# Performance work log

Measured on AMD Instinct MI355X. Metric: run time of the kernel, lower is better.

## Reference

```python
import jax, jax.numpy as jnp
import numpy as np

B, N, F_IN, F_OUT = 8, 2048, 64, 64
NEG = -9.0e15  # matches torch's -9000000000000000.0 mask value


def setup_inputs() -> dict:
    key = jax.random.key(0)
    ks = jax.random.split(key, 12)
    stdv1 = 1.0 / np.sqrt(F_IN)
    stdv2 = 1.0 / np.sqrt(2 * F_OUT)
    x = jax.random.normal(ks[0], (B, N, F_IN), dtype=jnp.float32)
    adj = jax.random.randint(ks[1], (B, N, N), 0, 2).astype(jnp.int32)
    identity = jnp.broadcast_to(jnp.eye(N, dtype=jnp.int32), (B, N, N))
    def unif(k, shape, s):
        return jax.random.uniform(k, shape, jnp.float32, -s, s)
    return {
        "x": x, "adj": adj, "identity": identity,
        "W1": unif(ks[2], (F_OUT, F_IN), stdv1), "b1": unif(ks[3], (F_OUT,), stdv1),
        "a1": unif(ks[4], (1, 2 * F_OUT), stdv2), "ab1": unif(ks[5], (1,), stdv2),
        "W2": unif(ks[6], (F_OUT, F_IN), stdv1), "b2": unif(ks[7], (F_OUT,), stdv1),
        "a2": unif(ks[8], (1, 2 * F_OUT), stdv2), "ab2": unif(ks[9], (1,), stdv2),
    }


def _gat_layer(x, mask, W, b, a, ab):
    # linear1
    h = jnp.einsum('bnf,of->bno', x, W) + b                     # [B,N,Fo]
    Fo = h.shape[-1]
    # linear2 on concat(h_i, h_j) decomposes: e_ij = relu(h_i.a1 + h_j.a2 + ab)
    s1 = h @ a[0, :Fo]                                          # [B,N]
    s2 = h @ a[0, Fo:]                                          # [B,N]
    e = jax.nn.relu(s1[:, :, None] + s2[:, None, :] + ab[0])    # [B,N,N]
    e = jnp.where(mask > 0, e, NEG)
    att = jax.nn.softmax(e, axis=2)                             # [B,N,N]
    return jnp.einsum('bnm,bmf->bnf', att, h)                   # dropout p=0 / eval


def reference(x, adj, identity, W1, b1, a1, ab1, W2, b2, a2, ab2):
    out1 = _gat_layer(x, adj, W1, b1, a1, ab1)
    out2 = _gat_layer(x, identity, W2, b2, a2, ab2)
    return out1 + out2
```

## Files before the change

kernel.cpp:

```cpp
#include <hip/hip_runtime.h>


#define DEVI __device__ __forceinline__

typedef __attribute__((ext_vector_type(8))) short short8;
typedef __attribute__((ext_vector_type(4))) float floatx4;

DEVI unsigned short f2bf(float x) {
    unsigned u = __builtin_bit_cast(unsigned, x);
    unsigned r = u + 0x7FFFu + ((u >> 16) & 1u);
    return (unsigned short)(r >> 16);
}

DEVI short8 pack8(const float* v) {
    short8 r;
#pragma unroll
    for (int i = 0; i < 8; ++i) r[i] = (short)f2bf(v[i]);
    return r;
}

DEVI unsigned cvt_pk_bf16(float lo, float hi) {
    unsigned r;
    asm("v_cvt_pk_bf16_f32 %0, %1, %2" : "=v"(r) : "v"(lo), "v"(hi));
    return r;
}

__global__ __launch_bounds__(256) void k_prep(
    const float* __restrict__ x, const float* __restrict__ W1,
    const float* __restrict__ b1, const float* __restrict__ a1,
    const float* __restrict__ ab1,
    unsigned short* __restrict__ hT1,
    float* __restrict__ t1,
    float* __restrict__ s2a)
{
    __shared__ __align__(16) unsigned short hstage[64][72];
    const int tid = threadIdx.x;
    const int w = tid >> 6, lane = tid & 63;
    const int g = lane >> 4, r15 = lane & 15;
    const int blockRow = blockIdx.x * 64;
    const int rowbase = blockRow + w * 16;

    float xa[8], xb[8];
    const float* xrow = x + (long)(rowbase + r15) * 64;
#pragma unroll
    for (int e = 0; e < 8; ++e) { xa[e] = xrow[g * 8 + e]; xb[e] = xrow[32 + g * 8 + e]; }
    short8 A0 = pack8(xa), A1 = pack8(xb);

    floatx4 acc[4];
#pragma unroll
    for (int nt = 0; nt < 4; ++nt) {
        float wa[8], wb[8];
        const float* wrow = W1 + (nt * 16 + r15) * 64;
#pragma unroll
        for (int e = 0; e < 8; ++e) { wa[e] = wrow[g * 8 + e]; wb[e] = wrow[32 + g * 8 + e]; }
        short8 B0 = pack8(wa), B1 = pack8(wb);
        floatx4 c = {0.f, 0.f, 0.f, 0.f};
        c = __builtin_amdgcn_mfma_f32_16x16x32_bf16(A0, B0, c, 0, 0, 0);
        c = __builtin_amdgcn_mfma_f32_16x16x32_bf16(A1, B1, c, 0, 0, 0);
        float bias = b1[nt * 16 + r15];
#pragma unroll
        for (int q = 0; q < 4; ++q) c[q] += bias;
        acc[nt] = c;
    }

    float a1lo[4], a1hi[4];
#pragma unroll
    for (int nt = 0; nt < 4; ++nt) {
        a1lo[nt] = a1[nt * 16 + r15];
        a1hi[nt] = a1[64 + nt * 16 + r15];
    }
    float s1q[4], s2q[4];
#pragma unroll
    for (int q = 0; q < 4; ++q) {
        float s1 = 0.f, s2 = 0.f;
#pragma unroll
        for (int nt = 0; nt < 4; ++nt) { s1 += acc[nt][q] * a1lo[nt]; s2 += acc[nt][q] * a1hi[nt]; }
#pragma unroll
        for (int m = 1; m < 16; m <<= 1) { s1 += __shfl_xor(s1, m); s2 += __shfl_xor(s2, m); }
        s1q[q] = s1; s2q[q] = s2;
    }
    if (r15 == 0) {
        float abv = ab1[0];
#pragma unroll
        for (int q = 0; q < 4; ++q) {
            t1[rowbase + 4 * g + q] = s1q[q] + abv;
            s2a[rowbase + 4 * g + q] = s2q[q];
        }
    }

#pragma unroll
    for (int nt = 0; nt < 4; ++nt)
#pragma unroll
        for (int q = 0; q < 4; ++q)
            hstage[nt * 16 + r15][w * 16 + 4 * g + q] = f2bf(acc[nt][q]);
    __syncthreads();
    {
        const int o = tid >> 2, seg = (tid & 3) * 16;
        const int bb = blockRow >> 11;
        const int ib = blockRow & 2047;
        unsigned short* dst = hT1 + ((long)(bb * 64 + o) * 2048) + ib + seg;
        uint4 v0 = *(const uint4*)&hstage[o][seg];
        uint4 v1 = *(const uint4*)&hstage[o][seg + 8];
        *(uint4*)dst = v0;
        *(uint4*)(dst + 8) = v1;
    }
}

__global__ __launch_bounds__(256, 1) void k_attn(
    const float* __restrict__ x, const int* __restrict__ adj,
    const float* __restrict__ W2, const float* __restrict__ b2,
    const unsigned short* __restrict__ hT1,
    const float* __restrict__ t1, const float* __restrict__ s2a,
    float* __restrict__ out)
{
    __shared__ __align__(16) unsigned short hl[4][8192];
    __shared__ __align__(16) unsigned short plds[4][16][72];

    const int tid = threadIdx.x;
    const int w = tid >> 6, lane = tid & 63;
    const int g = lane >> 4, r15 = lane & 15;
    const int bb = blockIdx.x & 7;
    const int it = blockIdx.x >> 3;
    const int rowbase = it * 64 + w * 16;

    const int fr8 = lane >> 3;
    const int fsl = (lane & 7) ^ (fr8 & 7);
    const int bs0 = g ^ (r15 & 7);
    const int bs1 = (4 + g) ^ (r15 & 7);

    unsigned short* hlw = &hl[4][0] - 8192 * (4 - w);
    unsigned short* pw = &plds[w][0][0];

    float tr4[4];
#pragma unroll
    for (int rr = 0; rr < 4; ++rr) tr4[rr] = t1[bb * 2048 + rowbase + rr * 4 + g];

    floatx4 acc[4];
#pragma unroll
    for (int nt = 0; nt < 4; ++nt) acc[nt] = (floatx4){0.f, 0.f, 0.f, 0.f};
    floatx4 acc5 = {0.f, 0.f, 0.f, 0.f};

    short8 ones;
#pragma unroll
    for (int i = 0; i < 8; ++i) ones[i] = (short)0x3F80;

    const int4* adjq = (const int4*)(adj + (long)(bb * 2048 + rowbase + g) * 2048) + r15;
    const float4* s2q4 = (const float4*)(s2a + (long)bb * 2048) + r15;
    const unsigned short* hTln = hT1 + (long)(bb * 64 + fr8) * 2048 + (lane & 7) * 8;

    int4 adjR[4][4];
    float4 s2R[4];
    uint4 hrg[2][8];

#define ADJ(c) do {                                                            \
        s2R[(c) & 3] = s2q4[(c) * 16];                                         \
        _Pragma("unroll")                                                      \
        for (int rr_ = 0; rr_ < 4; ++rr_)                                      \
            adjR[(c) & 3][rr_] = adjq[rr_ * 2048 + (c) * 16];                  \
    } while (0)

#define HTLOAD(c) do {                                                         \
        const unsigned short* s_ = hTln + (c) * 64;                            \
        _Pragma("unroll")                                                      \
        for (int k_ = 0; k_ < 8; ++k_)                                         \
            hrg[(c) & 1][k_] = *(const uint4*)(s_ + (long)k_ * 16384);         \
    } while (0)

#define HTSTORE(c) do {                                                        \
        _Pragma("unroll")                                                      \
        for (int k_ = 0; k_ < 8; ++k_)                                         \
            *(uint4*)&hlw[((c) & 1) * 4096 + (k_ * 8 + fr8) * 64 + fsl * 8]    \
                = hrg[(c) & 1][k_];                                            \
    } while (0)

#define COMPUTE(C) do {                                                        \
        const float4 s2v_ = s2R[(C) & 3];                                      \
        _Pragma("unroll")                                                      \
        for (int rr_ = 0; rr_ < 4; ++rr_) {                                    \
            float z0 = fmaxf(tr4[rr_] + s2v_.x, 0.f);                          \
            float z1 = fmaxf(tr4[rr_] + s2v_.y, 0.f);                          \
            float z2 = fmaxf(tr4[rr_] + s2v_.z, 0.f);                          \
            float z3 = fmaxf(tr4[rr_] + s2v_.w, 0.f);                          \
            float p0 = adjR[(C) & 3][rr_].x > 0 ? __expf(z0) : 0.f;            \
            float p1 = adjR[(C) & 3][rr_].y > 0 ? __expf(z1) : 0.f;            \
            float p2 = adjR[(C) & 3][rr_].z > 0 ? __expf(z2) : 0.f;            \
            float p3 = adjR[(C) & 3][rr_].w > 0 ? __expf(z3) : 0.f;            \
            uint2 u;                                                           \
            u.x = cvt_pk_bf16(p0, p1);                                         \
            u.y = cvt_pk_bf16(p2, p3);                                         \
            *(uint2*)&pw[(rr_ * 4 + g) * 72 + r15 * 4] = u;                    \
        }                                                                      \
        short8 a0 = *(const short8*)&pw[r15 * 72 + g * 8];                     \
        short8 a1 = *(const short8*)&pw[r15 * 72 + 32 + g * 8];                \
        const int bufo_ = ((C) & 1) * 4096;                                    \
        _Pragma("unroll")                                                      \
        for (int nt_ = 0; nt_ < 4; ++nt_) {                                    \
            short8 b0 = *(const short8*)&hlw[bufo_ + (nt_ * 16 + r15) * 64 + bs0 * 8]; \
            short8 b1 = *(const short8*)&hlw[bufo_ + (nt_ * 16 + r15) * 64 + bs1 * 8]; \
            acc[nt_] = __builtin_amdgcn_mfma_f32_16x16x32_bf16(a0, b0, acc[nt_], 0, 0, 0); \
            acc[nt_] = __builtin_amdgcn_mfma_f32_16x16x32_bf16(a1, b1, acc[nt_], 0, 0, 0); \
        }                                                                      \
        acc5 = __builtin_amdgcn_mfma_f32_16x16x32_bf16(a0, ones, acc5, 0, 0, 0); \
        acc5 = __builtin_amdgcn_mfma_f32_16x16x32_bf16(a1, ones, acc5, 0, 0, 0); \
    } while (0)

    ADJ(0); ADJ(1); ADJ(2);
    HTLOAD(0);
    HTSTORE(0);
    HTLOAD(1);

#pragma unroll
    for (int C = 0; C < 32; ++C) {
        if (C + 2 <= 31) HTLOAD(C + 2);
        if (C + 3 <= 31) ADJ(C + 3);
        if (C + 1 <= 31) HTSTORE(C + 1);
        COMPUTE(C);
    }

#undef COMPUTE
#undef HTSTORE
#undef HTLOAD
#undef ADJ

    float linv[4];
#pragma unroll
    for (int q = 0; q < 4; ++q) linv[q] = 1.0f / acc5[q];

    float xa[8], xb[8];
    const float* xrow = x + ((long)(bb * 2048 + rowbase + r15)) * 64;
#pragma unroll
    for (int e = 0; e < 8; ++e) { xa[e] = xrow[g * 8 + e]; xb[e] = xrow[32 + g * 8 + e]; }
    short8 A0 = pack8(xa), A1 = pack8(xb);
#pragma unroll
    for (int nt = 0; nt < 4; ++nt) {
        float wa[8], wb[8];
        const float* wrow2 = W2 + (nt * 16 + r15) * 64;
#pragma unroll
        for (int e = 0; e < 8; ++e) { wa[e] = wrow2[g * 8 + e]; wb[e] = wrow2[32 + g * 8 + e]; }
        short8 B0 = pack8(wa), B1 = pack8(wb);
        floatx4 c = {0.f, 0.f, 0.f, 0.f};
        c = __builtin_amdgcn_mfma_f32_16x16x32_bf16(A0, B0, c, 0, 0, 0);
        c = __builtin_amdgcn_mfma_f32_16x16x32_bf16(A1, B1, c, 0, 0, 0);
        float bias = b2[nt * 16 + r15];
#pragma unroll
        for (int q = 0; q < 4; ++q) {
            float val = acc[nt][q] * linv[q] + c[q] + bias;
            out[((long)(bb * 2048 + rowbase + 4 * g + q)) * 64 + nt * 16 + r15] = val;
        }
    }
}

extern "C" void kernel_launch(void* const* d_in, const int* in_sizes, int n_in,
                              void* d_out, int out_size, void* d_ws, size_t ws_size,
                              hipStream_t stream) {
    const float* x   = (const float*)d_in[0];
    const int*   adj = (const int*)d_in[1];
    const float* W1  = (const float*)d_in[3];
    const float* b1  = (const float*)d_in[4];
    const float* a1  = (const float*)d_in[5];
    const float* ab1 = (const float*)d_in[6];
    const float* W2  = (const float*)d_in[7];
    const float* b2  = (const float*)d_in[8];

    unsigned short* hT1 = (unsigned short*)d_ws;
    float* t1  = (float*)((char*)d_ws + (size_t)8 * 64 * 2048 * 2);
    float* s2a = t1 + 8 * 2048;

    k_prep<<<256, 256, 0, stream>>>(x, W1, b1, a1, ab1, hT1, t1, s2a);
    k_attn<<<256, 256, 0, stream>>>(x, adj, W2, b2, hT1, t1, s2a, (float*)d_out);
}
```

Baseline: 41.91 us.

## Split key range across four wave teams and factor exp into product

The attention kernel grows to 1024 threads per block. Four teams of four waves each take one quarter of the 2048 key columns and combine their partial accumulators through LDS at the end. The exponential is factored as exp(relu(a+b)) = max(exp(a)*exp(b), 1), so k_prep precomputes exp(t1) and exp(s2) and the inner loop uses one multiply and a max instead of an exp per element. The probability tile is now built directly in registers in the MFMA operand layout, which removes the LDS round trip, and adjacency is loaded row-per-lane. The costs are block-wide barriers every chunk, an extra reduction pass, and possible overflow of the exp product for large logits.

```diff
diff --git a/kernel.cpp b/kernel.cpp
--- a/kernel.cpp
+++ b/kernel.cpp
@@ -23,6 +23,13 @@
     unsigned r;
     asm("v_cvt_pk_bf16_f32 %0, %1, %2" : "=v"(r) : "v"(lo), "v"(hi));
     return r;
+}
+
+DEVI void team_sync() {
+    __builtin_amdgcn_sched_barrier(0);
+    asm volatile("s_waitcnt lgkmcnt(0)" ::: "memory");
+    __builtin_amdgcn_s_barrier();
+    __builtin_amdgcn_sched_barrier(0);
 }
 
 __global__ __launch_bounds__(256) void k_prep(
@@ -30,8 +37,8 @@
     const float* __restrict__ b1, const float* __restrict__ a1,
     const float* __restrict__ ab1,
     unsigned short* __restrict__ hT1,
-    float* __restrict__ t1,
-    float* __restrict__ s2a)
+    float* __restrict__ expt1,
+    float* __restrict__ expv)
 {
     __shared__ __align__(16) unsigned short hstage[64][72];
     const int tid = threadIdx.x;
@@ -83,8 +90,8 @@
         float abv = ab1[0];
 #pragma unroll
         for (int q = 0; q < 4; ++q) {
-            t1[rowbase + 4 * g + q] = s1q[q] + abv;
-            s2a[rowbase + 4 * g + q] = s2q[q];
+            expt1[rowbase + 4 * g + q] = __expf(s1q[q] + abv);
+            expv[rowbase + 4 * g + q]  = __expf(s2q[q]);
         }
     }
 
@@ -106,34 +113,28 @@
     }
 }
 
-__global__ __launch_bounds__(256, 1) void k_attn(
+__global__ __launch_bounds__(1024, 4) void k_attn(
     const float* __restrict__ x, const int* __restrict__ adj,
     const float* __restrict__ W2, const float* __restrict__ b2,
     const unsigned short* __restrict__ hT1,
-    const float* __restrict__ t1, const float* __restrict__ s2a,
+    const float* __restrict__ expt1, const float* __restrict__ expv,
     float* __restrict__ out)
 {
-    __shared__ __align__(16) unsigned short hl[4][8192];
-    __shared__ __align__(16) unsigned short plds[4][16][72];
+    __shared__ __align__(16) unsigned short hl[4][2][64][72];
+    __shared__ __align__(16) float vlds[2048];
 
     const int tid = threadIdx.x;
     const int w = tid >> 6, lane = tid & 63;
+    const int t = w >> 2, wrow = w & 3;
     const int g = lane >> 4, r15 = lane & 15;
     const int bb = blockIdx.x & 7;
     const int it = blockIdx.x >> 3;
-    const int rowbase = it * 64 + w * 16;
-
-    const int fr8 = lane >> 3;
-    const int fsl = (lane & 7) ^ (fr8 & 7);
-    const int bs0 = g ^ (r15 & 7);
-    const int bs1 = (4 + g) ^ (r15 & 7);
-
-    unsigned short* hlw = &hl[4][0] - 8192 * (4 - w);
-    unsigned short* pw = &plds[w][0][0];
-
-    float tr4[4];
-#pragma unroll
-    for (int rr = 0; rr < 4; ++rr) tr4[rr] = t1[bb * 2048 + rowbase + rr * 4 + g];
+    const int rowbase = it * 64 + wrow * 16;
+    const int jt0 = t * 8;
+
+    *(float2*)&vlds[tid * 2] = *(const float2*)&expv[bb * 2048 + tid * 2];
+
+    const float u = expt1[bb * 2048 + rowbase + r15];
 
     floatx4 acc[4];
 #pragma unroll
@@ -144,59 +145,68 @@
 #pragma unroll
     for (int i = 0; i < 8; ++i) ones[i] = (short)0x3F80;
 
-    const int4* adjq = (const int4*)(adj + (long)(bb * 2048 + rowbase + g) * 2048) + r15;
-    const float4* s2q4 = (const float4*)(s2a + (long)bb * 2048) + r15;
-    const unsigned short* hTln = hT1 + (long)(bb * 64 + fr8) * 2048 + (lane & 7) * 8;
-
-    int4 adjR[4][4];
-    float4 s2R[4];
-    uint4 hrg[2][8];
+    const int4* adjq = (const int4*)(adj + (long)(bb * 2048 + rowbase + r15) * 2048);
+
+    const int ttid = tid & 255;
+    const int so = ttid >> 2, sseg = (ttid & 3) * 16;
+    const unsigned short* hTsrc = hT1 + (long)(bb * 64 + so) * 2048 + sseg;
+    unsigned short* hldst0 = &hl[t][0][so][sseg];
+    unsigned short* hldst1 = &hl[t][1][so][sseg];
+
+    int4 adjR[2][4];
+    uint4 hrg[2][2];
 
 #define ADJ(c) do {                                                            \
-        s2R[(c) & 3] = s2q4[(c) * 16];                                         \
-        _Pragma("unroll")                                                      \
-        for (int rr_ = 0; rr_ < 4; ++rr_)                                      \
-            adjR[(c) & 3][rr_] = adjq[rr_ * 2048 + (c) * 16];                  \
+        const int base_ = (jt0 + (c)) * 16 + g * 2;                            \
+        adjR[(c) & 1][0] = adjq[base_];                                        \
+        adjR[(c) & 1][1] = adjq[base_ + 1];                                    \
+        adjR[(c) & 1][2] = adjq[base_ + 8];                                    \
+        adjR[(c) & 1][3] = adjq[base_ + 9];                                    \
     } while (0)
 
 #define HTLOAD(c) do {                                                         \
-        const unsigned short* s_ = hTln + (c) * 64;                            \
-        _Pragma("unroll")                                                      \
-        for (int k_ = 0; k_ < 8; ++k_)                                         \
-            hrg[(c) & 1][k_] = *(const uint4*)(s_ + (long)k_ * 16384);         \
+        const unsigned short* s_ = hTsrc + (jt0 + (c)) * 64;                   \
+        hrg[(c) & 1][0] = *(const uint4*)s_;                                   \
+        hrg[(c) & 1][1] = *(const uint4*)(s_ + 8);                             \
     } while (0)
 
 #define HTSTORE(c) do {                                                        \
-        _Pragma("unroll")                                                      \
-        for (int k_ = 0; k_ < 8; ++k_)                                         \
-            *(uint4*)&hlw[((c) & 1) * 4096 + (k_ * 8 + fr8) * 64 + fsl * 8]    \
-                = hrg[(c) & 1][k_];                                            \
+        unsigned short* d_ = ((c) & 1) ? hldst1 : hldst0;                      \
+        *(uint4*)d_ = hrg[(c) & 1][0];                                         \
+        *(uint4*)(d_ + 8) = hrg[(c) & 1][1];                                   \
     } while (0)
 
 #define COMPUTE(C) do {                                                        \
-        const float4 s2v_ = s2R[(C) & 3];                                      \
-        _Pragma("unroll")                                                      \
-        for (int rr_ = 0; rr_ < 4; ++rr_) {                                    \
-            float z0 = fmaxf(tr4[rr_] + s2v_.x, 0.f);                          \
-            float z1 = fmaxf(tr4[rr_] + s2v_.y, 0.f);                          \
-            float z2 = fmaxf(tr4[rr_] + s2v_.z, 0.f);                          \
-            float z3 = fmaxf(tr4[rr_] + s2v_.w, 0.f);                          \
-            float p0 = adjR[(C) & 3][rr_].x > 0 ? __expf(z0) : 0.f;            \
-            float p1 = adjR[(C) & 3][rr_].y > 0 ? __expf(z1) : 0.f;            \
-            float p2 = adjR[(C) & 3][rr_].z > 0 ? __expf(z2) : 0.f;            \
-            float p3 = adjR[(C) & 3][rr_].w > 0 ? __expf(z3) : 0.f;            \
-            uint2 u;                                                           \
-            u.x = cvt_pk_bf16(p0, p1);                                         \
-            u.y = cvt_pk_bf16(p2, p3);                                         \
-            *(uint2*)&pw[(rr_ * 4 + g) * 72 + r15 * 4] = u;                    \
-        }                                                                      \
-        short8 a0 = *(const short8*)&pw[r15 * 72 + g * 8];                     \
-        short8 a1 = *(const short8*)&pw[r15 * 72 + 32 + g * 8];                \
-        const int bufo_ = ((C) & 1) * 4096;                                    \
+        const int vb_ = (jt0 + (C)) * 64 + g * 8;                              \
+        float4 v0_ = *(const float4*)&vlds[vb_];                               \
+        float4 v1_ = *(const float4*)&vlds[vb_ + 4];                           \
+        float4 v2_ = *(const float4*)&vlds[vb_ + 32];                          \
+        float4 v3_ = *(const float4*)&vlds[vb_ + 36];                          \
+        int4 j0_ = adjR[(C) & 1][0], j1_ = adjR[(C) & 1][1];                   \
+        int4 j2_ = adjR[(C) & 1][2], j3_ = adjR[(C) & 1][3];                   \
+        uint4 au_, bu_;                                                        \
+        au_.x = cvt_pk_bf16(j0_.x > 0 ? fmaxf(u * v0_.x, 1.f) : 0.f,           \
+                            j0_.y > 0 ? fmaxf(u * v0_.y, 1.f) : 0.f);          \
+        au_.y = cvt_pk_bf16(j0_.z > 0 ? fmaxf(u * v0_.z, 1.f) : 0.f,           \
+                            j0_.w > 0 ? fmaxf(u * v0_.w, 1.f) : 0.f);          \
+        au_.z = cvt_pk_bf16(j1_.x > 0 ? fmaxf(u * v1_.x, 1.f) : 0.f,           \
+                            j1_.y > 0 ? fmaxf(u * v1_.y, 1.f) : 0.f);          \
+        au_.w = cvt_pk_bf16(j1_.z > 0 ? fmaxf(u * v1_.z, 1.f) : 0.f,           \
+                            j1_.w > 0 ? fmaxf(u * v1_.w, 1.f) : 0.f);          \
+        bu_.x = cvt_pk_bf16(j2_.x > 0 ? fmaxf(u * v2_.x, 1.f) : 0.f,           \
+                            j2_.y > 0 ? fmaxf(u * v2_.y, 1.f) : 0.f);          \
+        bu_.y = cvt_pk_bf16(j2_.z > 0 ? fmaxf(u * v2_.z, 1.f) : 0.f,           \
+                            j2_.w > 0 ? fmaxf(u * v2_.w, 1.f) : 0.f);          \
+        bu_.z = cvt_pk_bf16(j3_.x > 0 ? fmaxf(u * v3_.x, 1.f) : 0.f,           \
+                            j3_.y > 0 ? fmaxf(u * v3_.y, 1.f) : 0.f);          \
+        bu_.w = cvt_pk_bf16(j3_.z > 0 ? fmaxf(u * v3_.z, 1.f) : 0.f,           \
+                            j3_.w > 0 ? fmaxf(u * v3_.w, 1.f) : 0.f);          \
+        short8 a0 = __builtin_bit_cast(short8, au_);                           \
+        short8 a1 = __builtin_bit_cast(short8, bu_);                           \
         _Pragma("unroll")                                                      \
         for (int nt_ = 0; nt_ < 4; ++nt_) {                                    \
-            short8 b0 = *(const short8*)&hlw[bufo_ + (nt_ * 16 + r15) * 64 + bs0 * 8]; \
-            short8 b1 = *(const short8*)&hlw[bufo_ + (nt_ * 16 + r15) * 64 + bs1 * 8]; \
+            short8 b0 = *(const short8*)&hl[t][(C) & 1][nt_ * 16 + r15][g * 8];      \
+            short8 b1 = *(const short8*)&hl[t][(C) & 1][nt_ * 16 + r15][32 + g * 8]; \
             acc[nt_] = __builtin_amdgcn_mfma_f32_16x16x32_bf16(a0, b0, acc[nt_], 0, 0, 0); \
             acc[nt_] = __builtin_amdgcn_mfma_f32_16x16x32_bf16(a1, b1, acc[nt_], 0, 0, 0); \
         }                                                                      \
@@ -204,17 +214,19 @@
         acc5 = __builtin_amdgcn_mfma_f32_16x16x32_bf16(a1, ones, acc5, 0, 0, 0); \
     } while (0)
 
-    ADJ(0); ADJ(1); ADJ(2);
+    ADJ(0); ADJ(1);
     HTLOAD(0);
     HTSTORE(0);
     HTLOAD(1);
-
-#pragma unroll
-    for (int C = 0; C < 32; ++C) {
-        if (C + 2 <= 31) HTLOAD(C + 2);
-        if (C + 3 <= 31) ADJ(C + 3);
-        if (C + 1 <= 31) HTSTORE(C + 1);
+    team_sync();
+
+#pragma unroll
+    for (int C = 0; C < 8; ++C) {
+        if (C < 6) HTLOAD(C + 2);
+        if (C < 7) HTSTORE(C + 1);
         COMPUTE(C);
+        if (C < 6) ADJ(C + 2);
+        team_sync();
     }
 
 #undef COMPUTE
@@ -222,30 +234,58 @@
 #undef HTLOAD
 #undef ADJ
 
-    float linv[4];
-#pragma unroll
-    for (int q = 0; q < 4; ++q) linv[q] = 1.0f / acc5[q];
-
-    float xa[8], xb[8];
-    const float* xrow = x + ((long)(bb * 2048 + rowbase + r15)) * 64;
-#pragma unroll
-    for (int e = 0; e < 8; ++e) { xa[e] = xrow[g * 8 + e]; xb[e] = xrow[32 + g * 8 + e]; }
-    short8 A0 = pack8(xa), A1 = pack8(xb);
-#pragma unroll
-    for (int nt = 0; nt < 4; ++nt) {
-        float wa[8], wb[8];
-        const float* wrow2 = W2 + (nt * 16 + r15) * 64;
-#pragma unroll
-        for (int e = 0; e < 8; ++e) { wa[e] = wrow2[g * 8 + e]; wb[e] = wrow2[32 + g * 8 + e]; }
-        short8 B0 = pack8(wa), B1 = pack8(wb);
-        floatx4 c = {0.f, 0.f, 0.f, 0.f};
-        c = __builtin_amdgcn_mfma_f32_16x16x32_bf16(A0, B0, c, 0, 0, 0);
-        c = __builtin_amdgcn_mfma_f32_16x16x32_bf16(A1, B1, c, 0, 0, 0);
-        float bias = b2[nt * 16 + r15];
-#pragma unroll
-        for (int q = 0; q < 4; ++q) {
-            float val = acc[nt][q] * linv[q] + c[q] + bias;
-            out[((long)(bb * 2048 + rowbase + 4 * g + q)) * 64 + nt * 16 + r15] = val;
+    float* csh = (float*)&hl[0][0][0][0];
+    if (t > 0) {
+        const int wb = ((t - 1) * 4 + wrow) * 20;
+#pragma unroll
+        for (int nt = 0; nt < 4; ++nt)
+#pragma unroll
+            for (int q = 0; q < 4; ++q)
+                csh[(wb + nt * 4 + q) * 64 + lane] = acc[nt][q];
+#pragma unroll
+        for (int q = 0; q < 4; ++q)
+            csh[(wb + 16 + q) * 64 + lane] = acc5[q];
+    }
+    __syncthreads();
+
+    if (t == 0) {
+#pragma unroll
+        for (int ti = 0; ti < 3; ++ti) {
+            const int wb = (ti * 4 + wrow) * 20;
+#pragma unroll
+            for (int nt = 0; nt < 4; ++nt)
+#pragma unroll
+                for (int q = 0; q < 4; ++q)
+                    acc[nt][q] += csh[(wb + nt * 4 + q) * 64 + lane];
+#pragma unroll
+            for (int q = 0; q < 4; ++q)
+                acc5[q] += csh[(wb + 16 + q) * 64 + lane];
+        }
+        float linv[4];
+#pragma unroll
+        for (int q = 0; q < 4; ++q) linv[q] = 1.0f / acc5[q];
+
+        float xa[8], xb[8];
+        const float* xrow = x + ((long)(bb * 2048 + rowbase + r15)) * 64;
+#pragma unroll
+        for (int e = 0; e < 8; ++e) { xa[e] = xrow[g * 8 + e]; xb[e] = xrow[32 + g * 8 + e]; }
+        short8 A0 = pack8(xa), A1 = pack8(xb);
+#pragma unroll
+        for (int nt = 0; nt < 4; ++nt) {
+            float wa[8], wb[8];
+            const float* wrow2 = W2 + (nt * 16 + r15) * 64;
+#pragma unroll
+            for (int e = 0; e < 8; ++e) { wa[e] = wrow2[g * 8 + e]; wb[e] = wrow2[32 + g * 8 + e]; }
+            short8 B0 = pack8(wa), B1 = pack8(wb);
+            floatx4 c = {0.f, 0.f, 0.f, 0.f};
+            c = __builtin_amdgcn_mfma_f32_16x16x32_bf16(A0, B0, c, 0, 0, 0);
+            c = __builtin_amdgcn_mfma_f32_16x16x32_bf16(A1, B1, c, 0, 0, 0);
+            float bias = b2[nt * 16 + r15];
+#pragma unroll
+            for (int q = 0; q < 4; ++q) {
+                float val = acc[nt][q] * linv[q] + c[q] + bias;
+                out[((long)(bb * 2048 + rowbase + 4 * g + q)) * 64 + nt * 16 + r15] = val;
+            }
         }
     }
 }
@@ -263,9 +303,9 @@
     const float* b2  = (const float*)d_in[8];
 
     unsigned short* hT1 = (unsigned short*)d_ws;
-    float* t1  = (float*)((char*)d_ws + (size_t)8 * 64 * 2048 * 2);
-    float* s2a = t1 + 8 * 2048;
-
-    k_prep<<<256, 256, 0, stream>>>(x, W1, b1, a1, ab1, hT1, t1, s2a);
-    k_attn<<<256, 256, 0, stream>>>(x, adj, W2, b2, hT1, t1, s2a, (float*)d_out);
-}
+    float* expt1 = (float*)((char*)d_ws + (size_t)8 * 64 * 2048 * 2);
+    float* expv  = expt1 + 8 * 2048;
+
+    k_prep<<<256, 256, 0, stream>>>(x, W1, b1, a1, ab1, hT1, expt1, expv);
+    k_attn<<<256, 1024, 0, stream>>>(x, adj, W2, b2, hT1, expt1, expv, (float*)d_out);
+}
```

New measurement: 39.61 us, median of 2. 1.06x faster.
